# Kernel optimization log

Measured on AMD Instinct MI355X. Metric: run time of the kernel, lower is better.

## Reference

```python
import jax, jax.numpy as jnp
import numpy as np

N_NODES = 200000
N_EDGES = 4000000  # doubled (w2b + b2w), matches edge_weight param size
N_W2B = 2000000


def gcn_conv(x, W, b, src, dst, ew, n):
    # PyG GCNConv with add_self_loops=True, symmetric normalization.
    loop = jnp.arange(n)
    src_sl = jnp.concatenate([src, loop])
    dst_sl = jnp.concatenate([dst, loop])
    w_sl = jnp.concatenate([ew, jnp.ones((n,), ew.dtype)])  # self-loop weight 1
    deg = jax.ops.segment_sum(w_sl, dst_sl, num_segments=n)
    dinv = jnp.where(deg > 0, jax.lax.rsqrt(deg), 0.0)
    norm = dinv[src_sl] * w_sl * dinv[dst_sl]          # [E+N]
    xw = x @ W                                          # [N, out]
    msg = xw[src_sl] * norm[:, None]                    # [E+N, out]
    out = jax.ops.segment_sum(msg, dst_sl, num_segments=n)
    return out + b


def setup_inputs() -> dict:
    key = jax.random.key(0)
    ks = jax.random.split(key, 16)
    h1, h2, h3, h4, out = 8, 16, 32, 4, 3
    inp = 7

    def lin_init(k, fan_in, fan_out):
        bound = 1.0 / np.sqrt(fan_in)
        kw, kb = jax.random.split(k)
        W = jax.random.uniform(kw, (fan_in, fan_out), jnp.float32, -bound, bound)
        b = jax.random.uniform(kb, (fan_out,), jnp.float32, -bound, bound)
        return W, b

    x = jax.random.normal(ks[0], (N_NODES, inp), jnp.float32)
    edge_index = jax.random.randint(ks[1], (2, N_EDGES), 0, N_NODES, jnp.int64)
    w2b = jax.random.randint(ks[2], (2, N_W2B), 0, N_NODES, jnp.int64)
    edge_weight = jnp.ones((N_EDGES,), jnp.float32)  # Parameter init: ones

    W1, b1 = lin_init(ks[3], inp, h1)
    W2, b2 = lin_init(ks[4], h1, h2)
    W3, b3 = lin_init(ks[5], h2, h3)
    Wl1, bl1 = lin_init(ks[6], 2 * h3, h4)
    Wl2, bl2 = lin_init(ks[7], h4, out)

    return dict(x=x, edge_index=edge_index, w2b=w2b, edge_weight=edge_weight,
                W1=W1, b1=b1, W2=W2, b2=b2, W3=W3, b3=b3,
                Wl1=Wl1, bl1=bl1, Wl2=Wl2, bl2=bl2)


def reference(x, edge_index, w2b, edge_weight,
              W1, b1, W2, b2, W3, b3, Wl1, bl1, Wl2, bl2):
    n = x.shape[0]
    src, dst = edge_index[0], edge_index[1]
    ew = jax.nn.sigmoid(edge_weight)
    h = jax.nn.relu(gcn_conv(x, W1, b1, src, dst, ew, n))
    h = jax.nn.relu(gcn_conv(h, W2, b2, src, dst, ew, n))
    h = jax.nn.relu(gcn_conv(h, W3, b3, src, dst, ew, n))
    # fused gather-concat replacing the per-edge python loop
    concat = jnp.concatenate([h[w2b[0]], h[w2b[1]]], axis=-1)  # [E_w2b, 2*h3]
    hidden = concat @ Wl1 + bl1
    edge_pred = hidden @ Wl2 + bl2
    return edge_pred
```

## Files before the change

kernel.cpp:

```cpp
#include <hip/hip_runtime.h>
#include <hip/hip_bf16.h>
#include <hip/hip_fp16.h>


#define NB1 1024
#define NPB 256
#define MAXBINS 1024
#define LBINS 784
#define TILE 3907
#define QS 16384.0f
#define QINV (1.0f / 16384.0f)

typedef _Float16 h2 __attribute__((ext_vector_type(2)));
typedef _Float16 h4 __attribute__((ext_vector_type(4)));
typedef _Float16 h8 __attribute__((ext_vector_type(8)));

__device__ __forceinline__ float sigmoidf_(float x) {
    return 1.0f / (1.0f + __expf(-x));
}

__global__ void p1a_hist(const int* __restrict__ dst, int* __restrict__ bh,
                         int ne, int nbins, int chunk) {
    __shared__ int h[MAXBINS];
    for (int k = threadIdx.x; k < nbins; k += 256) h[k] = 0;
    __syncthreads();
    int base = blockIdx.x * chunk;
    int end = min(base + chunk, ne);
    int e = base + threadIdx.x;
    for (; e + 256 < end; e += 512) {
        int d0 = dst[e];
        int d1 = dst[e + 256];
        atomicAdd(&h[d0 >> 8], 1);
        atomicAdd(&h[d1 >> 8], 1);
    }
    if (e < end) atomicAdd(&h[dst[e] >> 8], 1);
    __syncthreads();
    for (int k = threadIdx.x; k < nbins; k += 256)
        bh[(size_t)k * NB1 + blockIdx.x] = h[k];
}

__global__ void s1_scan(int* __restrict__ bh, int* __restrict__ bintot) {
    __shared__ int sums[256];
    constexpr int W = NB1 / 256;
    int* row = bh + (size_t)blockIdx.x * NB1;
    int v[W];
    int s = 0;
#pragma unroll
    for (int j = 0; j < W; ++j) { v[j] = row[threadIdx.x * W + j]; s += v[j]; }
    sums[threadIdx.x] = s;
    __syncthreads();
    for (int o = 1; o < 256; o <<= 1) {
        int t = (threadIdx.x >= o) ? sums[threadIdx.x - o] : 0;
        __syncthreads();
        sums[threadIdx.x] += t;
        __syncthreads();
    }
    int excl = sums[threadIdx.x] - s;
#pragma unroll
    for (int j = 0; j < W; ++j) { row[threadIdx.x * W + j] = excl; excl += v[j]; }
    if (threadIdx.x == 255) bintot[blockIdx.x] = sums[255];
}

__global__ void s2_scan(const int* __restrict__ bintot, int* __restrict__ binbase,
                        int nbins, int ne) {
    __shared__ int tmp[1024];
    int tid = threadIdx.x;
    int v = (tid < nbins) ? bintot[tid] : 0;
    tmp[tid] = v;
    __syncthreads();
    for (int o = 1; o < 1024; o <<= 1) {
        int t = (tid >= o) ? tmp[tid - o] : 0;
        __syncthreads();
        tmp[tid] += t;
        __syncthreads();
    }
    if (tid < nbins) binbase[tid] = tmp[tid] - v;
    if (tid == 0) binbase[nbins] = ne;
}

__global__ void p1b_scatter(const int* __restrict__ src, const int* __restrict__ dst,
                            const float* __restrict__ ew, const int* __restrict__ bh,
                            const int* __restrict__ binbase,
                            unsigned long long* __restrict__ b64,
                            int ne, int nbins, int chunk) {
    __shared__ unsigned long long stage[TILE];
    __shared__ int hist[LBINS];
    __shared__ int boff[LBINS];
    __shared__ int cur[LBINS];
    __shared__ int wsum[4];
    int tid = threadIdx.x;
    int lane = tid & 63, wid = tid >> 6;
    for (int k = tid; k < nbins; k += 256)
        cur[k] = binbase[k] + bh[(size_t)k * NB1 + blockIdx.x];
    int t0 = blockIdx.x * chunk;
    int cnt = min(TILE, ne - t0);
    for (int k = tid; k < nbins; k += 256) hist[k] = 0;
    __syncthreads();
    {
        int j = tid;
        for (; j + 256 < cnt; j += 512) {
            int d0 = dst[t0 + j];
            int d1 = dst[t0 + j + 256];
            atomicAdd(&hist[d0 >> 8], 1);
            atomicAdd(&hist[d1 >> 8], 1);
        }
        if (j < cnt) atomicAdd(&hist[dst[t0 + j] >> 8], 1);
    }
    __syncthreads();
    int w0 = tid * 4;
    int lv[4];
    int ls = 0;
#pragma unroll
    for (int j = 0; j < 4; ++j) {
        lv[j] = (w0 + j < nbins) ? hist[w0 + j] : 0;
        ls += lv[j];
    }
    int s = ls;
    for (int o = 1; o < 64; o <<= 1) {
        int t = __shfl_up(s, o, 64);
        if (lane >= o) s += t;
    }
    if (lane == 63) wsum[wid] = s;
    __syncthreads();
    int wpre = 0;
    for (int w = 0; w < wid; ++w) wpre += wsum[w];
    int excl = wpre + s - ls;
#pragma unroll
    for (int j = 0; j < 4; ++j) {
        if (w0 + j < nbins) { boff[w0 + j] = excl; excl += lv[j]; }
    }
    __syncthreads();
    {
        int j = tid;
        for (; j + 256 < cnt; j += 512) {
            int e0 = t0 + j, e1 = t0 + j + 256;
            int d0 = dst[e0], d1 = dst[e1];
            float wq0 = sigmoidf_(ew[e0]);
            float wq1 = sigmoidf_(ew[e1]);
            int q0 = (int)fminf(wq0 * QS + 0.5f, 16383.0f);
            int q1 = (int)fminf(wq1 * QS + 0.5f, 16383.0f);
            unsigned long long v0 =
                (unsigned long long)((unsigned)src[e0] | ((unsigned)q0 << 18))
                | ((unsigned long long)(d0 & 255) << 32)
                | ((unsigned long long)(d0 >> 8) << 40);
            unsigned long long v1 =
                (unsigned long long)((unsigned)src[e1] | ((unsigned)q1 << 18))
                | ((unsigned long long)(d1 & 255) << 32)
                | ((unsigned long long)(d1 >> 8) << 40);
            int p0 = atomicAdd(&boff[d0 >> 8], 1);
            int p1 = atomicAdd(&boff[d1 >> 8], 1);
            stage[p0] = v0;
            stage[p1] = v1;
        }
        if (j < cnt) {
            int e0 = t0 + j;
            int d0 = dst[e0];
            float wq0 = sigmoidf_(ew[e0]);
            int q0 = (int)fminf(wq0 * QS + 0.5f, 16383.0f);
            unsigned long long v0 =
                (unsigned long long)((unsigned)src[e0] | ((unsigned)q0 << 18))
                | ((unsigned long long)(d0 & 255) << 32)
                | ((unsigned long long)(d0 >> 8) << 40);
            stage[atomicAdd(&boff[d0 >> 8], 1)] = v0;
        }
    }
    __syncthreads();
    for (int j = tid; j < cnt; j += 256) {
        unsigned long long v = stage[j];
        int b = (int)(v >> 40);
        b64[cur[b] + (j - (boff[b] - hist[b]))] = v;
    }
}

__global__ void p2_build(const unsigned long long* __restrict__ b64,
                         const int* __restrict__ binbase, unsigned* __restrict__ edata,
                         int* __restrict__ C, float* __restrict__ dinv,
                         const float* __restrict__ x, const float* __restrict__ W1,
                         _Float16* __restrict__ g0, int n, int ne, int nbins) {
    __shared__ int cnt[NPB];
    __shared__ int curs[NPB];
    __shared__ unsigned qsum[NPB];
    __shared__ float Ws[56];
    __shared__ int wsum[4];
    if (threadIdx.x < 56) Ws[threadIdx.x] = W1[threadIdx.x];
    int b = blockIdx.x;
    int E0 = binbase[b], E1 = binbase[b + 1];
    int tid = threadIdx.x;
    int lane = tid & 63, wid = tid >> 6;
    cnt[tid] = 0;
    qsum[tid] = 0;
    __syncthreads();
    {
        int k = E0 + tid;
        for (; k + 256 < E1; k += 512) {
            unsigned long long a = b64[k];
            unsigned long long c = b64[k + 256];
            atomicAdd(&cnt[(int)((a >> 32) & 0xFF)], 1);
            atomicAdd(&cnt[(int)((c >> 32) & 0xFF)], 1);
        }
        if (k < E1)
            atomicAdd(&cnt[(int)((b64[k] >> 32) & 0xFF)], 1);
    }
    __syncthreads();
    int v = cnt[tid];
    int s = v;
    for (int o = 1; o < 64; o <<= 1) {
        int t = __shfl_up(s, o, 64);
        if (lane >= o) s += t;
    }
    if (lane == 63) wsum[wid] = s;
    __syncthreads();
    int wpre = 0;
    for (int w = 0; w < wid; ++w) wpre += wsum[w];
    int excl = wpre + s - v;
    curs[tid] = E0 + excl;
    int node = b * NPB + tid;
    if (node < n) C[node] = E0 + excl;
    if (b == 0 && tid == 0) C[n] = ne;
    __syncthreads();
    {
        int k = E0 + tid;
        for (; k + 256 < E1; k += 512) {
            unsigned long long a = b64[k];
            unsigned long long c = b64[k + 256];
            int dla = (int)((a >> 32) & 0xFF);
            int dlc = (int)((c >> 32) & 0xFF);
            int pa = atomicAdd(&curs[dla], 1);
            int pc = atomicAdd(&curs[dlc], 1);
            edata[pa] = (unsigned)(a & 0xFFFFFFFFu);
            edata[pc] = (unsigned)(c & 0xFFFFFFFFu);
            atomicAdd(&qsum[dla], (unsigned)((a >> 18) & 0x3FFFu));
            atomicAdd(&qsum[dlc], (unsigned)((c >> 18) & 0x3FFFu));
        }
        if (k < E1) {
            unsigned long long a = b64[k];
            int dla = (int)((a >> 32) & 0xFF);
            int pa = atomicAdd(&curs[dla], 1);
            edata[pa] = (unsigned)(a & 0xFFFFFFFFu);
            atomicAdd(&qsum[dla], (unsigned)((a >> 18) & 0x3FFFu));
        }
    }
    __syncthreads();
    if (node < n) {
        float dv = rsqrtf((float)qsum[tid] * QINV + 1.0f);
        dinv[node] = dv;
        float xi[7];
#pragma unroll
        for (int k = 0; k < 7; ++k) xi[k] = x[(size_t)node * 7 + k];
        h8 r;
#pragma unroll
        for (int o = 0; o < 8; ++o) {
            float acc = 0.0f;
#pragma unroll
            for (int k = 0; k < 7; ++k) acc = fmaf(xi[k], Ws[k * 8 + o], acc);
            r[o] = (_Float16)(acc * dv);
        }
        *reinterpret_cast<h8*>(g0 + (size_t)node * 8) = r;
    }
}

__global__ void gather1_kernel(const _Float16* __restrict__ g, const float* __restrict__ dinv,
                               const int* __restrict__ C, const unsigned* __restrict__ edata,
                               const float* __restrict__ b1, _Float16* __restrict__ out, int n) {
    __shared__ float bs[8];
    if (threadIdx.x < 8) bs[threadIdx.x] = b1[threadIdx.x];
    __syncthreads();
    long long t = (long long)blockIdx.x * blockDim.x + threadIdx.x;
    int i = (int)(t >> 3);
    int l8 = (int)(t & 7);
    if (i >= n) return;
    int beg = C[i], end = C[i + 1];
    float acc[8] = {0.f, 0.f, 0.f, 0.f, 0.f, 0.f, 0.f, 0.f};
    if (l8 == 0) {
        h8 r = *reinterpret_cast<const h8*>(g + (size_t)i * 8);
#pragma unroll
        for (int j = 0; j < 8; ++j) acc[j] = (float)r[j];
    }
    int k = beg + l8;
    for (; k + 8 < end; k += 16) {
        unsigned v0 = edata[k];
        unsigned v1 = edata[k + 8];
        h8 r0 = *reinterpret_cast<const h8*>(g + (size_t)(v0 & 0x3FFFFu) * 8);
        h8 r1 = *reinterpret_cast<const h8*>(g + (size_t)(v1 & 0x3FFFFu) * 8);
        float w0 = (float)(v0 >> 18) * QINV;
        float w1 = (float)(v1 >> 18) * QINV;
#pragma unroll
        for (int j = 0; j < 8; ++j) acc[j] = fmaf((float)r0[j], w0, acc[j]);
#pragma unroll
        for (int j = 0; j < 8; ++j) acc[j] = fmaf((float)r1[j], w1, acc[j]);
    }
    if (k < end) {
        unsigned v = edata[k];
        float w = (float)(v >> 18) * QINV;
        h8 r = *reinterpret_cast<const h8*>(g + (size_t)(v & 0x3FFFFu) * 8);
#pragma unroll
        for (int j = 0; j < 8; ++j) acc[j] = fmaf((float)r[j], w, acc[j]);
    }
    bool t4 = (l8 & 4) != 0, t2 = (l8 & 2) != 0, t1 = (l8 & 1) != 0;
    float s4[4];
#pragma unroll
    for (int j = 0; j < 4; ++j) {
        float keep = t4 ? acc[4 + j] : acc[j];
        float send = t4 ? acc[j] : acc[4 + j];
        s4[j] = keep + __shfl_xor(send, 4, 64);
    }
    float s2[2];
#pragma unroll
    for (int j = 0; j < 2; ++j) {
        float keep = t2 ? s4[2 + j] : s4[j];
        float send = t2 ? s4[j] : s4[2 + j];
        s2[j] = keep + __shfl_xor(send, 2, 64);
    }
    float keep = t1 ? s2[1] : s2[0];
    float send = t1 ? s2[0] : s2[1];
    float s = keep + __shfl_xor(send, 1, 64);
    float dv = dinv[i];
    out[(size_t)i * 8 + l8] = (_Float16)(dv * fmaxf(dv * s + bs[l8], 0.0f));
}

__global__ void gather2_kernel(const _Float16* __restrict__ g, const float* __restrict__ dinv,
                               const int* __restrict__ C, const unsigned* __restrict__ edata,
                               const float* __restrict__ W2, const float* __restrict__ b2,
                               _Float16* __restrict__ out, int n) {
    __shared__ float Ws[128];
    __shared__ float bs[16];
    if (threadIdx.x < 128) Ws[threadIdx.x] = W2[threadIdx.x];
    if (threadIdx.x < 16) bs[threadIdx.x] = b2[threadIdx.x];
    __syncthreads();
    long long t = (long long)blockIdx.x * blockDim.x + threadIdx.x;
    int i = (int)(t >> 3);
    int l8 = (int)(t & 7);
    if (i >= n) return;
    int beg = C[i], end = C[i + 1];
    float acc[8] = {0.f, 0.f, 0.f, 0.f, 0.f, 0.f, 0.f, 0.f};
    if (l8 == 0) {
        h8 r = *reinterpret_cast<const h8*>(g + (size_t)i * 8);
#pragma unroll
        for (int j = 0; j < 8; ++j) acc[j] = (float)r[j];
    }
    int k = beg + l8;
    for (; k + 8 < end; k += 16) {
        unsigned v0 = edata[k];
        unsigned v1 = edata[k + 8];
        h8 r0 = *reinterpret_cast<const h8*>(g + (size_t)(v0 & 0x3FFFFu) * 8);
        h8 r1 = *reinterpret_cast<const h8*>(g + (size_t)(v1 & 0x3FFFFu) * 8);
        float w0 = (float)(v0 >> 18) * QINV;
        float w1 = (float)(v1 >> 18) * QINV;
#pragma unroll
        for (int j = 0; j < 8; ++j) acc[j] = fmaf((float)r0[j], w0, acc[j]);
#pragma unroll
        for (int j = 0; j < 8; ++j) acc[j] = fmaf((float)r1[j], w1, acc[j]);
    }
    if (k < end) {
        unsigned v = edata[k];
        float w = (float)(v >> 18) * QINV;
        h8 r = *reinterpret_cast<const h8*>(g + (size_t)(v & 0x3FFFFu) * 8);
#pragma unroll
        for (int j = 0; j < 8; ++j) acc[j] = fmaf((float)r[j], w, acc[j]);
    }
#pragma unroll
    for (int j = 0; j < 8; ++j) {
        acc[j] += __shfl_xor(acc[j], 1, 64);
        acc[j] += __shfl_xor(acc[j], 2, 64);
        acc[j] += __shfl_xor(acc[j], 4, 64);
    }
    float dv = dinv[i];
    float raw[8];
#pragma unroll
    for (int j = 0; j < 8; ++j) raw[j] = acc[j] * dv;
    int o0 = l8 * 2;
    h2 o2;
#pragma unroll
    for (int jo = 0; jo < 2; ++jo) {
        int o = o0 + jo;
        float h = bs[o];
#pragma unroll
        for (int k2 = 0; k2 < 8; ++k2) h = fmaf(raw[k2], Ws[k2 * 16 + o], h);
        o2[jo] = (_Float16)(dv * fmaxf(h, 0.0f));
    }
    *reinterpret_cast<h2*>(out + (size_t)i * 16 + o0) = o2;
}

__global__ void gather3_kernel(const _Float16* __restrict__ g, const float* __restrict__ dinv,
                               const int* __restrict__ C, const unsigned* __restrict__ edata,
                               _Float16* __restrict__ raw3, int n) {
    long long t = (long long)blockIdx.x * blockDim.x + threadIdx.x;
    int i = (int)(t >> 3);
    int l8 = (int)(t & 7);
    if (i >= n) return;
    int beg = C[i], end = C[i + 1];
    float acc[16];
#pragma unroll
    for (int j = 0; j < 16; ++j) acc[j] = 0.0f;
    if (l8 == 0) {
        h8 r0 = *reinterpret_cast<const h8*>(g + (size_t)i * 16);
        h8 r1 = *reinterpret_cast<const h8*>(g + (size_t)i * 16 + 8);
#pragma unroll
        for (int j = 0; j < 8; ++j) { acc[j] = (float)r0[j]; acc[8 + j] = (float)r1[j]; }
    }
    int k = beg + l8;
    for (; k + 8 < end; k += 16) {
        unsigned v0 = edata[k];
        unsigned v1 = edata[k + 8];
        size_t i0 = (size_t)(v0 & 0x3FFFFu) * 16;
        size_t i1 = (size_t)(v1 & 0x3FFFFu) * 16;
        h8 a0 = *reinterpret_cast<const h8*>(g + i0);
        h8 a1 = *reinterpret_cast<const h8*>(g + i0 + 8);
        h8 c0 = *reinterpret_cast<const h8*>(g + i1);
        h8 c1 = *reinterpret_cast<const h8*>(g + i1 + 8);
        float w0 = (float)(v0 >> 18) * QINV;
        float w1 = (float)(v1 >> 18) * QINV;
#pragma unroll
        for (int j = 0; j < 8; ++j) acc[j] = fmaf((float)a0[j], w0, acc[j]);
#pragma unroll
        for (int j = 0; j < 8; ++j) acc[8 + j] = fmaf((float)a1[j], w0, acc[8 + j]);
#pragma unroll
        for (int j = 0; j < 8; ++j) acc[j] = fmaf((float)c0[j], w1, acc[j]);
#pragma unroll
        for (int j = 0; j < 8; ++j) acc[8 + j] = fmaf((float)c1[j], w1, acc[8 + j]);
    }
    if (k < end) {
        unsigned v = edata[k];
        size_t i0 = (size_t)(v & 0x3FFFFu) * 16;
        h8 a0 = *reinterpret_cast<const h8*>(g + i0);
        h8 a1 = *reinterpret_cast<const h8*>(g + i0 + 8);
        float w = (float)(v >> 18) * QINV;
#pragma unroll
        for (int j = 0; j < 8; ++j) acc[j] = fmaf((float)a0[j], w, acc[j]);
#pragma unroll
        for (int j = 0; j < 8; ++j) acc[8 + j] = fmaf((float)a1[j], w, acc[8 + j]);
    }
    bool t4 = (l8 & 4) != 0, t2 = (l8 & 2) != 0, t1 = (l8 & 1) != 0;
    float s8[8];
#pragma unroll
    for (int j = 0; j < 8; ++j) {
        float keep = t4 ? acc[8 + j] : acc[j];
        float send = t4 ? acc[j] : acc[8 + j];
        s8[j] = keep + __shfl_xor(send, 4, 64);
    }
    float s4[4];
#pragma unroll
    for (int j = 0; j < 4; ++j) {
        float keep = t2 ? s8[4 + j] : s8[j];
        float send = t2 ? s8[j] : s8[4 + j];
        s4[j] = keep + __shfl_xor(send, 2, 64);
    }
    float s2[2];
#pragma unroll
    for (int j = 0; j < 2; ++j) {
        float keep = t1 ? s4[2 + j] : s4[j];
        float send = t1 ? s4[j] : s4[2 + j];
        s2[j] = keep + __shfl_xor(send, 1, 64);
    }
    float dv = dinv[i];
    h2 o2;
    o2[0] = (_Float16)(s2[0] * dv);
    o2[1] = (_Float16)(s2[1] * dv);
    *reinterpret_cast<h2*>(raw3 + (size_t)i * 16 + l8 * 2) = o2;
}

__global__ void dense3_kernel(const _Float16* __restrict__ raw3,
                              const float* __restrict__ W3, const float* __restrict__ b3,
                              const float* __restrict__ Wl1, const float* __restrict__ bl1,
                              const float* __restrict__ Wl2, const float* __restrict__ bl2,
                              _Float16* __restrict__ pqh, int n) {
    __shared__ __align__(16) float WsT[512];
    __shared__ float bs[32];
    __shared__ float wfs[192];
    __shared__ float bfs[3];
    for (int t = threadIdx.x; t < 512; t += 256) {
        int k = t >> 5, o = t & 31;
        WsT[o * 16 + k] = W3[t];
    }
    if (threadIdx.x < 32) bs[threadIdx.x] = b3[threadIdx.x];
    if (threadIdx.x < 192) {
        int f = threadIdx.x / 3, j = threadIdx.x % 3;
        float a = 0.0f;
#pragma unroll
        for (int k = 0; k < 4; ++k) a = fmaf(Wl1[f * 4 + k], Wl2[k * 3 + j], a);
        wfs[threadIdx.x] = a;
    }
    if (threadIdx.x < 3) {
        float a = bl2[threadIdx.x];
#pragma unroll
        for (int k = 0; k < 4; ++k) a = fmaf(bl1[k], Wl2[k * 3 + threadIdx.x], a);
        bfs[threadIdx.x] = a;
    }
    __syncthreads();
    int i = blockIdx.x * 256 + threadIdx.x;
    if (i >= n) return;
    h8 r0 = *reinterpret_cast<const h8*>(raw3 + (size_t)i * 16);
    h8 r1 = *reinterpret_cast<const h8*>(raw3 + (size_t)i * 16 + 8);
    float raw[16];
#pragma unroll
    for (int j = 0; j < 8; ++j) { raw[j] = (float)r0[j]; raw[8 + j] = (float)r1[j]; }
    float p0 = bfs[0], p1 = bfs[1], p2 = bfs[2];
    float q0 = 0.0f, q1 = 0.0f, q2 = 0.0f;
#pragma unroll
    for (int o = 0; o < 32; ++o) {
        const float4* w4 = reinterpret_cast<const float4*>(WsT + o * 16);
        float4 wa = w4[0], wb = w4[1], wc = w4[2], wd = w4[3];
        float h = bs[o];
        h = fmaf(raw[0], wa.x, h);  h = fmaf(raw[1], wa.y, h);
        h = fmaf(raw[2], wa.z, h);  h = fmaf(raw[3], wa.w, h);
        h = fmaf(raw[4], wb.x, h);  h = fmaf(raw[5], wb.y, h);
        h = fmaf(raw[6], wb.z, h);  h = fmaf(raw[7], wb.w, h);
        h = fmaf(raw[8], wc.x, h);  h = fmaf(raw[9], wc.y, h);
        h = fmaf(raw[10], wc.z, h); h = fmaf(raw[11], wc.w, h);
        h = fmaf(raw[12], wd.x, h); h = fmaf(raw[13], wd.y, h);
        h = fmaf(raw[14], wd.z, h); h = fmaf(raw[15], wd.w, h);
        h = fmaxf(h, 0.0f);
        p0 = fmaf(h, wfs[o * 3 + 0], p0);
        p1 = fmaf(h, wfs[o * 3 + 1], p1);
        p2 = fmaf(h, wfs[o * 3 + 2], p2);
        q0 = fmaf(h, wfs[(32 + o) * 3 + 0], q0);
        q1 = fmaf(h, wfs[(32 + o) * 3 + 1], q1);
        q2 = fmaf(h, wfs[(32 + o) * 3 + 2], q2);
    }
    h8 o8;
    o8[0] = (_Float16)p0; o8[1] = (_Float16)p1; o8[2] = (_Float16)p2; o8[3] = (_Float16)0.0f;
    o8[4] = (_Float16)q0; o8[5] = (_Float16)q1; o8[6] = (_Float16)q2; o8[7] = (_Float16)0.0f;
    *reinterpret_cast<h8*>(pqh + (size_t)i * 8) = o8;
}

__global__ void head_kernel(const int* __restrict__ w2b, const _Float16* __restrict__ pqh,
                            float* __restrict__ out, int nw) {
    int e = blockIdx.x * blockDim.x + threadIdx.x;
    if (e >= nw) return;
    int a = w2b[e];
    int b = w2b[(size_t)nw + e];
    h4 P = *reinterpret_cast<const h4*>(pqh + (size_t)a * 8);
    h4 Q = *reinterpret_cast<const h4*>(pqh + (size_t)b * 8 + 4);
    out[(size_t)e * 3 + 0] = (float)P[0] + (float)Q[0];
    out[(size_t)e * 3 + 1] = (float)P[1] + (float)Q[1];
    out[(size_t)e * 3 + 2] = (float)P[2] + (float)Q[2];
}

extern "C" void kernel_launch(void* const* d_in, const int* in_sizes, int n_in,
                              void* d_out, int out_size, void* d_ws, size_t ws_size,
                              hipStream_t stream) {
    const float* x   = (const float*)d_in[0];
    const int* eidx  = (const int*)d_in[1];
    const int* w2b   = (const int*)d_in[2];
    const float* ew  = (const float*)d_in[3];
    const float* W1  = (const float*)d_in[4];
    const float* b1  = (const float*)d_in[5];
    const float* W2  = (const float*)d_in[6];
    const float* b2  = (const float*)d_in[7];
    const float* W3  = (const float*)d_in[8];
    const float* b3  = (const float*)d_in[9];
    const float* Wl1 = (const float*)d_in[10];
    const float* bl1 = (const float*)d_in[11];
    const float* Wl2 = (const float*)d_in[12];
    const float* bl2 = (const float*)d_in[13];
    float* out = (float*)d_out;

    const int n  = in_sizes[0] / 7;
    const int ne = in_sizes[1] / 2;
    const int nw = in_sizes[2] / 2;
    const int* src = eidx;
    const int* dst = eidx + ne;

    const int nbins = (n + NPB - 1) / NPB;
    const int chunk = (ne + NB1 - 1) / NB1;

    float*     ws      = (float*)d_ws;
    float*     dinv    = ws;
    int*       C       = (int*)(ws + n);
    unsigned*  edata   = (unsigned*)(ws + 2 * (size_t)n + 16);
    int*       bh      = (int*)(edata + ne);
    int*       bintot  = bh + (size_t)nbins * NB1;
    int*       binbase = bintot + MAXBINS;
    _Float16*  g0      = (_Float16*)(binbase + MAXBINS);
    float*     bregion = (float*)(g0 + (size_t)n * 8);
    unsigned long long* b64 = (unsigned long long*)bregion;
    _Float16*  g1      = (_Float16*)bregion;
    _Float16*  g2      = (_Float16*)(bregion + 4 * (size_t)n);
    _Float16*  pqh     = (_Float16*)(bregion + 12 * (size_t)n);
    _Float16*  raw3    = (_Float16*)(bregion + 16 * (size_t)n);

    const int Bl = 256;
    auto blks = [&](long long t) { return (int)((t + Bl - 1) / Bl); };
    const int nb8 = blks((long long)n * 8);

    p1a_hist<<<NB1, Bl, 0, stream>>>(dst, bh, ne, nbins, chunk);
    s1_scan<<<nbins, Bl, 0, stream>>>(bh, bintot);
    s2_scan<<<1, 1024, 0, stream>>>(bintot, binbase, nbins, ne);
    p1b_scatter<<<NB1, Bl, 0, stream>>>(src, dst, ew, bh, binbase, b64, ne, nbins, chunk);
    p2_build<<<nbins, Bl, 0, stream>>>(b64, binbase, edata, C, dinv, x, W1, g0, n, ne, nbins);

    gather1_kernel<<<nb8, Bl, 0, stream>>>(g0, dinv, C, edata, b1, g1, n);
    gather2_kernel<<<nb8, Bl, 0, stream>>>(g1, dinv, C, edata, W2, b2, g2, n);
    gather3_kernel<<<nb8, Bl, 0, stream>>>(g2, dinv, C, edata, raw3, n);
    dense3_kernel<<<blks(n), Bl, 0, stream>>>(raw3, W3, b3, Wl1, bl1, Wl2, bl2, pqh, n);

    head_kernel<<<blks(nw), Bl, 0, stream>>>(w2b, pqh, out, nw);
}
```

Baseline: 331.6 us.

## Compute per-node degree and weight sums with global atomics during histogram pass

Moves per-destination degree counting and quantized weight-sum accumulation into the first histogram pass using global atomics on zeroed arrays. CSR offsets, dinv and the first-layer transform are then computed in a separate per-bin kernel before the scatter. This lets the second build pass skip its counting sweep over b64. The head kernel is also widened to two edges per thread with vector loads and stores. In exchange it adds a zeroing kernel and 8M scattered global atomics over 200K nodes, which may contend or cost more than the removed shared-memory pass.

```diff
diff --git a/kernel.cpp b/kernel.cpp
--- a/kernel.cpp
+++ b/kernel.cpp
@@ -19,8 +19,14 @@
     return 1.0f / (1.0f + __expf(-x));
 }
 
-__global__ void p1a_hist(const int* __restrict__ dst, int* __restrict__ bh,
-                         int ne, int nbins, int chunk) {
+__global__ void zero_kernel(int* __restrict__ p, int nwords) {
+    int i = blockIdx.x * 256 + threadIdx.x;
+    if (i < nwords) p[i] = 0;
+}
+
+__global__ void p1a_hist(const int* __restrict__ dst, const float* __restrict__ ew,
+                         int* __restrict__ bh, int* __restrict__ deg,
+                         int* __restrict__ qsumI, int ne, int nbins, int chunk) {
     __shared__ int h[MAXBINS];
     for (int k = threadIdx.x; k < nbins; k += 256) h[k] = 0;
     __syncthreads();
@@ -30,10 +36,22 @@
     for (; e + 256 < end; e += 512) {
         int d0 = dst[e];
         int d1 = dst[e + 256];
+        int q0 = (int)fminf(sigmoidf_(ew[e]) * QS + 0.5f, 16383.0f);
+        int q1 = (int)fminf(sigmoidf_(ew[e + 256]) * QS + 0.5f, 16383.0f);
         atomicAdd(&h[d0 >> 8], 1);
         atomicAdd(&h[d1 >> 8], 1);
-    }
-    if (e < end) atomicAdd(&h[dst[e] >> 8], 1);
+        atomicAdd(&deg[d0], 1);
+        atomicAdd(&deg[d1], 1);
+        atomicAdd(&qsumI[d0], q0);
+        atomicAdd(&qsumI[d1], q1);
+    }
+    if (e < end) {
+        int d0 = dst[e];
+        int q0 = (int)fminf(sigmoidf_(ew[e]) * QS + 0.5f, 16383.0f);
+        atomicAdd(&h[d0 >> 8], 1);
+        atomicAdd(&deg[d0], 1);
+        atomicAdd(&qsumI[d0], q0);
+    }
     __syncthreads();
     for (int k = threadIdx.x; k < nbins; k += 256)
         bh[(size_t)k * NB1 + blockIdx.x] = h[k];
@@ -76,6 +94,48 @@
     }
     if (tid < nbins) binbase[tid] = tmp[tid] - v;
     if (tid == 0) binbase[nbins] = ne;
+}
+
+__global__ void d2c_offsets(const int* __restrict__ deg, const int* __restrict__ qsumI,
+                            const int* __restrict__ binbase, int* __restrict__ C,
+                            float* __restrict__ dinv, const float* __restrict__ x,
+                            const float* __restrict__ W1, _Float16* __restrict__ g0,
+                            int n, int ne) {
+    __shared__ float Ws[56];
+    __shared__ int wsum[4];
+    int tid = threadIdx.x, lane = tid & 63, wid = tid >> 6;
+    if (tid < 56) Ws[tid] = W1[tid];
+    int b = blockIdx.x;
+    int node = b * NPB + tid;
+    int v = (node < n) ? deg[node] : 0;
+    int s = v;
+    for (int o = 1; o < 64; o <<= 1) {
+        int t = __shfl_up(s, o, 64);
+        if (lane >= o) s += t;
+    }
+    if (lane == 63) wsum[wid] = s;
+    __syncthreads();
+    int wpre = 0;
+    for (int w = 0; w < wid; ++w) wpre += wsum[w];
+    int excl = binbase[b] + wpre + s - v;
+    if (node < n) C[node] = excl;
+    if (b == 0 && tid == 0) C[n] = ne;
+    if (node < n) {
+        float dv = rsqrtf((float)qsumI[node] * QINV + 1.0f);
+        dinv[node] = dv;
+        float xi[7];
+#pragma unroll
+        for (int k = 0; k < 7; ++k) xi[k] = x[(size_t)node * 7 + k];
+        h8 r;
+#pragma unroll
+        for (int o = 0; o < 8; ++o) {
+            float acc = 0.0f;
+#pragma unroll
+            for (int k = 0; k < 7; ++k) acc = fmaf(xi[k], Ws[k * 8 + o], acc);
+            r[o] = (_Float16)(acc * dv);
+        }
+        *reinterpret_cast<h8*>(g0 + (size_t)node * 8) = r;
+    }
 }
 
 __global__ void p1b_scatter(const int* __restrict__ src, const int* __restrict__ dst,
@@ -172,90 +232,40 @@
     }
 }
 
-__global__ void p2_build(const unsigned long long* __restrict__ b64,
-                         const int* __restrict__ binbase, unsigned* __restrict__ edata,
-                         int* __restrict__ C, float* __restrict__ dinv,
-                         const float* __restrict__ x, const float* __restrict__ W1,
-                         _Float16* __restrict__ g0, int n, int ne, int nbins) {
-    __shared__ int cnt[NPB];
+__global__ void p2_scatter(const unsigned long long* __restrict__ b64,
+                           const int* __restrict__ binbase, const int* __restrict__ C,
+                           unsigned* __restrict__ edata, int n, int ne) {
     __shared__ int curs[NPB];
-    __shared__ unsigned qsum[NPB];
-    __shared__ float Ws[56];
-    __shared__ int wsum[4];
-    if (threadIdx.x < 56) Ws[threadIdx.x] = W1[threadIdx.x];
     int b = blockIdx.x;
+    int tid = threadIdx.x;
     int E0 = binbase[b], E1 = binbase[b + 1];
-    int tid = threadIdx.x;
-    int lane = tid & 63, wid = tid >> 6;
-    cnt[tid] = 0;
-    qsum[tid] = 0;
-    __syncthreads();
-    {
-        int k = E0 + tid;
-        for (; k + 256 < E1; k += 512) {
-            unsigned long long a = b64[k];
-            unsigned long long c = b64[k + 256];
-            atomicAdd(&cnt[(int)((a >> 32) & 0xFF)], 1);
-            atomicAdd(&cnt[(int)((c >> 32) & 0xFF)], 1);
-        }
-        if (k < E1)
-            atomicAdd(&cnt[(int)((b64[k] >> 32) & 0xFF)], 1);
-    }
-    __syncthreads();
-    int v = cnt[tid];
-    int s = v;
-    for (int o = 1; o < 64; o <<= 1) {
-        int t = __shfl_up(s, o, 64);
-        if (lane >= o) s += t;
-    }
-    if (lane == 63) wsum[wid] = s;
-    __syncthreads();
-    int wpre = 0;
-    for (int w = 0; w < wid; ++w) wpre += wsum[w];
-    int excl = wpre + s - v;
-    curs[tid] = E0 + excl;
     int node = b * NPB + tid;
-    if (node < n) C[node] = E0 + excl;
-    if (b == 0 && tid == 0) C[n] = ne;
-    __syncthreads();
-    {
-        int k = E0 + tid;
-        for (; k + 256 < E1; k += 512) {
-            unsigned long long a = b64[k];
-            unsigned long long c = b64[k + 256];
-            int dla = (int)((a >> 32) & 0xFF);
-            int dlc = (int)((c >> 32) & 0xFF);
-            int pa = atomicAdd(&curs[dla], 1);
-            int pc = atomicAdd(&curs[dlc], 1);
-            edata[pa] = (unsigned)(a & 0xFFFFFFFFu);
-            edata[pc] = (unsigned)(c & 0xFFFFFFFFu);
-            atomicAdd(&qsum[dla], (unsigned)((a >> 18) & 0x3FFFu));
-            atomicAdd(&qsum[dlc], (unsigned)((c >> 18) & 0x3FFFu));
-        }
-        if (k < E1) {
-            unsigned long long a = b64[k];
-            int dla = (int)((a >> 32) & 0xFF);
-            int pa = atomicAdd(&curs[dla], 1);
-            edata[pa] = (unsigned)(a & 0xFFFFFFFFu);
-            atomicAdd(&qsum[dla], (unsigned)((a >> 18) & 0x3FFFu));
-        }
-    }
-    __syncthreads();
-    if (node < n) {
-        float dv = rsqrtf((float)qsum[tid] * QINV + 1.0f);
-        dinv[node] = dv;
-        float xi[7];
-#pragma unroll
-        for (int k = 0; k < 7; ++k) xi[k] = x[(size_t)node * 7 + k];
-        h8 r;
-#pragma unroll
-        for (int o = 0; o < 8; ++o) {
-            float acc = 0.0f;
-#pragma unroll
-            for (int k = 0; k < 7; ++k) acc = fmaf(xi[k], Ws[k * 8 + o], acc);
-            r[o] = (_Float16)(acc * dv);
-        }
-        *reinterpret_cast<h8*>(g0 + (size_t)node * 8) = r;
+    curs[tid] = (node < n) ? C[node] : ne;
+    __syncthreads();
+    int k = E0 + tid;
+    for (; k + 768 < E1; k += 1024) {
+        unsigned long long a = b64[k];
+        unsigned long long c = b64[k + 256];
+        unsigned long long d = b64[k + 512];
+        unsigned long long f = b64[k + 768];
+        int dla = (int)((a >> 32) & 0xFF);
+        int dlc = (int)((c >> 32) & 0xFF);
+        int dld = (int)((d >> 32) & 0xFF);
+        int dlf = (int)((f >> 32) & 0xFF);
+        int pa = atomicAdd(&curs[dla], 1);
+        int pc = atomicAdd(&curs[dlc], 1);
+        int pd = atomicAdd(&curs[dld], 1);
+        int pf = atomicAdd(&curs[dlf], 1);
+        edata[pa] = (unsigned)(a & 0xFFFFFFFFu);
+        edata[pc] = (unsigned)(c & 0xFFFFFFFFu);
+        edata[pd] = (unsigned)(d & 0xFFFFFFFFu);
+        edata[pf] = (unsigned)(f & 0xFFFFFFFFu);
+    }
+    for (; k < E1; k += 256) {
+        unsigned long long a = b64[k];
+        int dla = (int)((a >> 32) & 0xFF);
+        int pa = atomicAdd(&curs[dla], 1);
+        edata[pa] = (unsigned)(a & 0xFFFFFFFFu);
     }
 }
 
@@ -525,15 +535,36 @@
 
 __global__ void head_kernel(const int* __restrict__ w2b, const _Float16* __restrict__ pqh,
                             float* __restrict__ out, int nw) {
-    int e = blockIdx.x * blockDim.x + threadIdx.x;
-    if (e >= nw) return;
-    int a = w2b[e];
-    int b = w2b[(size_t)nw + e];
-    h4 P = *reinterpret_cast<const h4*>(pqh + (size_t)a * 8);
-    h4 Q = *reinterpret_cast<const h4*>(pqh + (size_t)b * 8 + 4);
-    out[(size_t)e * 3 + 0] = (float)P[0] + (float)Q[0];
-    out[(size_t)e * 3 + 1] = (float)P[1] + (float)Q[1];
-    out[(size_t)e * 3 + 2] = (float)P[2] + (float)Q[2];
+    int t = blockIdx.x * 256 + threadIdx.x;
+    int e0 = t * 2;
+    if (e0 >= nw) return;
+    if (e0 + 1 < nw) {
+        int2 A = *reinterpret_cast<const int2*>(w2b + e0);
+        int2 B = *reinterpret_cast<const int2*>(w2b + (size_t)nw + e0);
+        h4 P0 = *reinterpret_cast<const h4*>(pqh + (size_t)A.x * 8);
+        h4 Q0 = *reinterpret_cast<const h4*>(pqh + (size_t)B.x * 8 + 4);
+        h4 P1 = *reinterpret_cast<const h4*>(pqh + (size_t)A.y * 8);
+        h4 Q1 = *reinterpret_cast<const h4*>(pqh + (size_t)B.y * 8 + 4);
+        float* o = out + (size_t)e0 * 3;
+        float2 w01, w23, w45;
+        w01.x = (float)P0[0] + (float)Q0[0];
+        w01.y = (float)P0[1] + (float)Q0[1];
+        w23.x = (float)P0[2] + (float)Q0[2];
+        w23.y = (float)P1[0] + (float)Q1[0];
+        w45.x = (float)P1[1] + (float)Q1[1];
+        w45.y = (float)P1[2] + (float)Q1[2];
+        *reinterpret_cast<float2*>(o) = w01;
+        *reinterpret_cast<float2*>(o + 2) = w23;
+        *reinterpret_cast<float2*>(o + 4) = w45;
+    } else {
+        int a = w2b[e0];
+        int b = w2b[(size_t)nw + e0];
+        h4 P = *reinterpret_cast<const h4*>(pqh + (size_t)a * 8);
+        h4 Q = *reinterpret_cast<const h4*>(pqh + (size_t)b * 8 + 4);
+        out[(size_t)e0 * 3 + 0] = (float)P[0] + (float)Q[0];
+        out[(size_t)e0 * 3 + 1] = (float)P[1] + (float)Q[1];
+        out[(size_t)e0 * 3 + 2] = (float)P[2] + (float)Q[2];
+    }
 }
 
 extern "C" void kernel_launch(void* const* d_in, const int* in_sizes, int n_in,
@@ -571,7 +602,9 @@
     int*       bh      = (int*)(edata + ne);
     int*       bintot  = bh + (size_t)nbins * NB1;
     int*       binbase = bintot + MAXBINS;
-    _Float16*  g0      = (_Float16*)(binbase + MAXBINS);
+    int*       deg     = binbase + MAXBINS + 16;
+    int*       qsumI   = deg + n;
+    _Float16*  g0      = (_Float16*)(qsumI + n);
     float*     bregion = (float*)(g0 + (size_t)n * 8);
     unsigned long long* b64 = (unsigned long long*)bregion;
     _Float16*  g1      = (_Float16*)bregion;
@@ -583,16 +616,18 @@
     auto blks = [&](long long t) { return (int)((t + Bl - 1) / Bl); };
     const int nb8 = blks((long long)n * 8);
 
-    p1a_hist<<<NB1, Bl, 0, stream>>>(dst, bh, ne, nbins, chunk);
+    zero_kernel<<<blks(2 * (long long)n), Bl, 0, stream>>>(deg, 2 * n);
+    p1a_hist<<<NB1, Bl, 0, stream>>>(dst, ew, bh, deg, qsumI, ne, nbins, chunk);
     s1_scan<<<nbins, Bl, 0, stream>>>(bh, bintot);
     s2_scan<<<1, 1024, 0, stream>>>(bintot, binbase, nbins, ne);
+    d2c_offsets<<<nbins, Bl, 0, stream>>>(deg, qsumI, binbase, C, dinv, x, W1, g0, n, ne);
     p1b_scatter<<<NB1, Bl, 0, stream>>>(src, dst, ew, bh, binbase, b64, ne, nbins, chunk);
-    p2_build<<<nbins, Bl, 0, stream>>>(b64, binbase, edata, C, dinv, x, W1, g0, n, ne, nbins);
+    p2_scatter<<<nbins, Bl, 0, stream>>>(b64, binbase, C, edata, n, ne);
 
     gather1_kernel<<<nb8, Bl, 0, stream>>>(g0, dinv, C, edata, b1, g1, n);
     gather2_kernel<<<nb8, Bl, 0, stream>>>(g1, dinv, C, edata, W2, b2, g2, n);
     gather3_kernel<<<nb8, Bl, 0, stream>>>(g2, dinv, C, edata, raw3, n);
     dense3_kernel<<<blks(n), Bl, 0, stream>>>(raw3, W3, b3, Wl1, bl1, Wl2, bl2, pqh, n);
 
-    head_kernel<<<blks(nw), Bl, 0, stream>>>(w2b, pqh, out, nw);
-}
+    head_kernel<<<blks((nw + 1) / 2), Bl, 0, stream>>>(w2b, pqh, out, nw);
+}
```

Measured after the change: 617.2 us. 86.1% more time.
